# Performance work log

Measured on AMD Instinct MI355X. Metric: run time of the kernel, lower is better.

The kernel has to match this reference:

```python
import jax, jax.numpy as jnp
import numpy as np

D_MODEL = 1024
N_HEADS = 16
HEAD_DIM = D_MODEL // N_HEADS
N_EXPERTS = 4
HIDDEN = 4 * D_MODEL
B, T = 1, 2048


def _apply_rope(x, sin, cos):
    # x: [..., D]; sin/cos broadcastable to [..., D/2]
    x1, x2 = x[..., ::2], x[..., 1::2]
    r1 = x1 * cos - x2 * sin
    r2 = x1 * sin + x2 * cos
    return jnp.stack((r1, r2), axis=-1).reshape(x.shape)


def setup_inputs() -> dict:
    key = jax.random.key(0)
    ks = jax.random.split(key, 16)
    s = 0.02
    d, E, Hd = D_MODEL, N_EXPERTS, HIDDEN
    return {
        "x": jax.random.normal(ks[0], (B, T, d), dtype=jnp.float32),
        "w_dw": jax.random.normal(ks[1], (d, 3), dtype=jnp.float32) * s,      # depthwise conv k=3
        "w_pw": jax.random.normal(ks[2], (d, d), dtype=jnp.float32) * s,      # pointwise conv [out,in]
        "w_qkv": jax.random.normal(ks[3], (3 * d, d), dtype=jnp.float32) * s,  # [out,in]
        "w_o": jax.random.normal(ks[4], (d, d), dtype=jnp.float32) * s,
        "w_gate": jax.random.normal(ks[5], (d, d), dtype=jnp.float32) * s,
        "b_gate": jnp.zeros((d,), dtype=jnp.float32),
        "ln_g": jnp.ones((d,), dtype=jnp.float32),
        "ln_b": jnp.zeros((d,), dtype=jnp.float32),
        "w_moe_gate": jax.random.normal(ks[6], (E, d), dtype=jnp.float32) * s,  # Linear no bias [out,in]
        "w1": jax.random.normal(ks[7], (E, Hd, d), dtype=jnp.float32) * s,
        "b1": jnp.zeros((E, Hd), dtype=jnp.float32),
        "w2": jax.random.normal(ks[8], (E, d, Hd), dtype=jnp.float32) * s,
        "b2": jnp.zeros((E, d), dtype=jnp.float32),
    }


def reference(x, w_dw, w_pw, w_qkv, w_o, w_gate, b_gate, ln_g, ln_b,
              w_moe_gate, w1, b1, w2, b2):
    Bv, Tv, d = x.shape
    H, Dh = N_HEADS, HEAD_DIM
    dt = x.dtype

    # --- causal conv mixer (depthwise k=3, causal left pad 2, then pointwise) ---
    xp = jnp.pad(x, ((0, 0), (2, 0), (0, 0)))
    y = (xp[:, 0:Tv] * w_dw[:, 0] + xp[:, 1:Tv + 1] * w_dw[:, 1]
         + xp[:, 2:Tv + 2] * w_dw[:, 2])
    y = jnp.einsum('btd,ed->bte', y, w_pw)
    x = x + y

    # --- qkv projection + split heads ---
    qkv = jnp.einsum('btd,ed->bte', x, w_qkv).reshape(Bv, Tv, 3, H, Dh)
    q, k, v = qkv[:, :, 0], qkv[:, :, 1], qkv[:, :, 2]

    # --- RoPE (head_dim even) ---
    inv_freq = 1.0 / (10000.0 ** (jnp.arange(0, Dh, 2, dtype=dt) / Dh))
    pos = jnp.arange(Tv, dtype=dt)
    theta = pos[:, None] * inv_freq[None, :]                 # [T, Dh/2]
    sin = jnp.sin(theta)[None, :, None, :]                   # [1,T,1,Dh/2]
    cos = jnp.cos(theta)[None, :, None, :]
    q = _apply_rope(q, sin, cos)
    k = _apply_rope(k, sin, cos)

    # --- linear attention via full kv outer-product cumsum ---
    q_phi = jax.nn.elu(q) + 1.0
    k_phi = jax.nn.elu(k) + 1.0
    kv = k_phi[..., :, None] * v[..., None, :]               # [B,T,H,D,D]
    kv_prefix = jnp.cumsum(kv, axis=1)
    k_prefix = jnp.cumsum(k_phi, axis=1)
    num = jnp.einsum('bthd,bthdm->bthm', q_phi, kv_prefix)
    denom = jnp.sum(q_phi * k_prefix, axis=-1, keepdims=True)
    attn = num / (denom + 1e-6)
    attn = attn.reshape(Bv, Tv, d)
    attn = jnp.einsum('btd,ed->bte', attn, w_o)

    # --- delta-gated residual (dropout = identity in eval) ---
    delta = x - jnp.concatenate([x[:, :1], x[:, :-1]], axis=1)
    gate = jax.nn.sigmoid(jnp.einsum('btd,ed->bte', delta, w_gate) + b_gate)
    x = x + gate * attn

    # --- LayerNorm + dense MoE FFN ---
    mu = jnp.mean(x, axis=-1, keepdims=True)
    var = jnp.mean((x - mu) ** 2, axis=-1, keepdims=True)
    h = (x - mu) / jnp.sqrt(var + 1e-5) * ln_g + ln_b

    gw = jax.nn.softmax(jnp.einsum('btd,ed->bte', h, w_moe_gate), axis=-1)  # [B,T,E]
    hid = jax.nn.silu(jnp.einsum('btd,efd->btef', h, w1) + b1)              # [B,T,E,Hd]
    eo = jnp.einsum('btef,edf->bted', hid, w2) + b2                          # [B,T,E,d]
    ffn = jnp.einsum('bte,bted->btd', gw, eo)
    return x + ffn
```

## Files before the change

### kernel.cpp

```cpp
#include <hip/hip_runtime.h>
#include <hip/hip_bf16.h>

#define TSEQ 2048
#define DM   1024
#define NHD  16
#define DHD  64
#define NEXP 4
#define HIDN 4096
#define NMOE (NEXP*HIDN)
#define CHK  128
#define NCHK (TSEQ/CHK)

typedef __attribute__((ext_vector_type(8))) short          bf16x8_v;
typedef __attribute__((ext_vector_type(4))) float          f32x4_v;
typedef __attribute__((ext_vector_type(4))) unsigned short us4_v;

__device__ __forceinline__ unsigned short bfbits(float f) {
  __hip_bfloat16 h = __float2bfloat16(f);
  return __builtin_bit_cast(unsigned short, h);
}
__device__ __forceinline__ float bf2f(unsigned short u) {
  return __uint_as_float(((unsigned)u) << 16);
}
__device__ __forceinline__ float wave_sum(float v) {
  #pragma unroll
  for (int o = 32; o; o >>= 1) v += __shfl_xor(v, o, 64);
  return v;
}
__device__ __forceinline__ void gl_lds16(const void* g, void* l) {
  __builtin_amdgcn_global_load_lds((const __attribute__((address_space(1))) void*)g,
                                   (__attribute__((address_space(3))) void*)l, 16, 0, 0);
}

__global__ __launch_bounds__(256) void cvt_bf16(const float* __restrict__ in,
                                                unsigned short* __restrict__ out, int n4) {
  int i = blockIdx.x * 256 + threadIdx.x;
  if (i >= n4) return;
  float4 v = ((const float4*)in)[i];
  us4_v o; o.x = bfbits(v.x); o.y = bfbits(v.y); o.z = bfbits(v.z); o.w = bfbits(v.w);
  ((us4_v*)out)[i] = o;
}

__global__ __launch_bounds__(256) void conv_dw(const float* __restrict__ x,
                                               const float* __restrict__ w_dw,
                                               unsigned short* __restrict__ y_bf) {
  int i = blockIdx.x * 256 + threadIdx.x;
  int c = i & (DM - 1);
  int t = i >> 10;
  float a = (t >= 2) ? x[i - 2 * DM] : 0.f;
  float b = (t >= 1) ? x[i - DM]     : 0.f;
  float d = x[i];
  float y = a * w_dw[c * 3] + b * w_dw[c * 3 + 1] + d * w_dw[c * 3 + 2];
  y_bf[i] = bfbits(y);
}

template <int EPI>
__global__ __launch_bounds__(256, 2) void gemm128s(
    const unsigned short* __restrict__ A, const unsigned short* __restrict__ A2,
    const unsigned short* __restrict__ B, const unsigned short* __restrict__ B2,
    float* __restrict__ Cf, float* __restrict__ Cf2,
    unsigned short* __restrict__ Cbf, const float* __restrict__ ex0,
    int lda, int ldb, int K, int ldc)
{
  if (EPI == 0) { if (blockIdx.z) { A = A2; B = B2; Cf = Cf2; } }

  __shared__ unsigned short As[2][128][64];
  __shared__ unsigned short Bs[2][128][64];

  const int nwg = gridDim.x * gridDim.y;
  const int bidl = blockIdx.y * gridDim.x + blockIdx.x;
  const int chunk = nwg >> 3;
  const int swz = (bidl & 7) * chunk + (bidl >> 3);
  const int ntn = gridDim.y;
  const int rest = swz >> 3;
  const int m0 = ((rest / ntn) * 8 + (swz & 7)) << 7;
  const int n0 = (rest % ntn) << 7;

  const int tid = threadIdx.x;
  const int srow = tid >> 3;
  const int scol = (tid & 7) << 3;
  const int scsw = (((tid & 7) ^ ((tid >> 3) & 7)) << 3);
  const unsigned short* gA = A + (size_t)(m0 + srow) * lda + scsw;
  const unsigned short* gB = B + (size_t)(n0 + srow) * ldb + scsw;

  auto stage = [&](int k0, int b) {
    #pragma unroll
    for (int i = 0; i < 4; i++)
      gl_lds16(gA + (size_t)(i * 32) * lda + k0, &As[b][i * 32 + srow][scol]);
    #pragma unroll
    for (int i = 0; i < 4; i++)
      gl_lds16(gB + (size_t)(i * 32) * ldb + k0, &Bs[b][i * 32 + srow][scol]);
  };

  const int lane = tid & 63, wv = tid >> 6;
  const int wr = (wv >> 1) << 6, wc = (wv & 1) << 6;
  const int fr = lane & 15, kreg = lane >> 4, r4 = kreg << 2;
  const int c0 = ((kreg) ^ (lane & 7)) << 3;
  const int c1 = ((4 + kreg) ^ (lane & 7)) << 3;

  f32x4_v acc[4][4] = {};

  stage(0, 0);
  const int nt = K >> 6;
  for (int t = 0; t < nt; t++) {
    const int p = t & 1;
    if (t + 1 < nt) {
      stage((t + 1) << 6, p ^ 1);
      asm volatile("s_waitcnt vmcnt(8)" ::: "memory");
    } else {
      asm volatile("s_waitcnt vmcnt(0)" ::: "memory");
    }
    __builtin_amdgcn_s_barrier();
    __builtin_amdgcn_sched_barrier(0);
    bf16x8_v af[4][2], bfm[4][2];
    #pragma unroll
    for (int m = 0; m < 4; m++) {
      af[m][0] = *(const bf16x8_v*)&As[p][wr + m * 16 + fr][c0];
      af[m][1] = *(const bf16x8_v*)&As[p][wr + m * 16 + fr][c1];
    }
    #pragma unroll
    for (int n = 0; n < 4; n++) {
      bfm[n][0] = *(const bf16x8_v*)&Bs[p][wc + n * 16 + fr][c0];
      bfm[n][1] = *(const bf16x8_v*)&Bs[p][wc + n * 16 + fr][c1];
    }
    __builtin_amdgcn_s_setprio(1);
    #pragma unroll
    for (int m = 0; m < 4; m++)
      #pragma unroll
      for (int n = 0; n < 4; n++) {
        acc[m][n] = __builtin_amdgcn_mfma_f32_16x16x32_bf16(af[m][0], bfm[n][0], acc[m][n], 0, 0, 0);
        acc[m][n] = __builtin_amdgcn_mfma_f32_16x16x32_bf16(af[m][1], bfm[n][1], acc[m][n], 0, 0, 0);
      }
    __builtin_amdgcn_s_setprio(0);
    __builtin_amdgcn_s_barrier();
  }

  #pragma unroll
  for (int m = 0; m < 4; m++)
    #pragma unroll
    for (int n = 0; n < 4; n++)
      #pragma unroll
      for (int j = 0; j < 4; j++) {
        int grow = m0 + wr + m * 16 + r4 + j;
        int gcol = n0 + wc + n * 16 + fr;
        size_t off = (size_t)grow * ldc + gcol;
        if (EPI == 0) {
          Cf[off] = acc[m][n][j];
        } else {
          float s = acc[m][n][j] + ex0[off];
          Cf[off] = s; Cbf[off] = bfbits(s);
        }
      }
}

template <int EPI>
__global__ __launch_bounds__(512, 1) void gemm256(
    const unsigned short* __restrict__ A, const unsigned short* __restrict__ B,
    float* __restrict__ Cf, unsigned short* __restrict__ Cbf,
    const float* __restrict__ ex0, const float* __restrict__ ex1,
    int lda, int ldb, int K, int ldc, int kPerZ)
{
  if (EPI == 1) {
    int ko = blockIdx.z * kPerZ;
    A += ko;
    B += (size_t)(ko >> 12) * DM * HIDN + (ko & 4095);
    K = kPerZ;
  }

  __shared__ unsigned short As[2][256][64];
  __shared__ unsigned short Bs[2][256][64];

  int bidl = blockIdx.y * gridDim.x + blockIdx.x;
  int chunk = (gridDim.x * gridDim.y) >> 3;
  int swz = (bidl & 7) * chunk + (bidl >> 3);
  int m0 = (swz & 7) << 8, n0 = (swz >> 3) << 8;

  const int tid = threadIdx.x;
  const int srow = tid >> 3;
  const int scol = (tid & 7) << 3;
  const int scsw = (((tid & 7) ^ ((tid >> 3) & 7)) << 3);
  const unsigned short* gA = A + (size_t)(m0 + srow) * lda + scsw;
  const unsigned short* gB = B + (size_t)(n0 + srow) * ldb + scsw;

  auto stageA = [&](int k0, int b) {
    #pragma unroll
    for (int i = 0; i < 4; i++)
      gl_lds16(gA + (size_t)(i * 64) * lda + k0, &As[b][i * 64 + srow][scol]);
  };
  auto stageB = [&](int k0, int b) {
    #pragma unroll
    for (int i = 0; i < 4; i++)
      gl_lds16(gB + (size_t)(i * 64) * ldb + k0, &Bs[b][i * 64 + srow][scol]);
  };

  const int lane = tid & 63, wv = tid >> 6;
  const int wm = wv >> 2, wn = wv & 3;
  const int fr = lane & 15;
  const int kreg = lane >> 4, r4 = kreg << 2;
  const int c0 = ((kreg) ^ (lane & 7)) << 3;
  const int c1 = ((4 + kreg) ^ (lane & 7)) << 3;

  f32x4_v acc[8][4] = {};
  bf16x8_v a0[4][2], a1[4][2], bb[2][2];

  stageA(0, 0); stageB(0, 0);
  const int nt = K >> 6;
  for (int t = 0; t < nt; t++) {
    const int p = t & 1;
    if (t + 1 < nt) {
      stageA((t + 1) << 6, p ^ 1);
      asm volatile("s_waitcnt vmcnt(4)" ::: "memory");
    } else {
      asm volatile("s_waitcnt vmcnt(0)" ::: "memory");
    }
    __builtin_amdgcn_s_barrier();
    __builtin_amdgcn_sched_barrier(0);
    #pragma unroll
    for (int m = 0; m < 4; m++) {
      a0[m][0] = *(const bf16x8_v*)&As[p][wm * 128 + m * 16 + fr][c0];
      a0[m][1] = *(const bf16x8_v*)&As[p][wm * 128 + m * 16 + fr][c1];
    }
    #pragma unroll
    for (int n = 0; n < 2; n++) {
      bb[n][0] = *(const bf16x8_v*)&Bs[p][wn * 64 + n * 16 + fr][c0];
      bb[n][1] = *(const bf16x8_v*)&Bs[p][wn * 64 + n * 16 + fr][c1];
    }
    __builtin_amdgcn_s_setprio(1);
    #pragma unroll
    for (int m = 0; m < 4; m++)
      #pragma unroll
      for (int n = 0; n < 2; n++) {
        acc[m][n] = __builtin_amdgcn_mfma_f32_16x16x32_bf16(a0[m][0], bb[n][0], acc[m][n], 0, 0, 0);
        acc[m][n] = __builtin_amdgcn_mfma_f32_16x16x32_bf16(a0[m][1], bb[n][1], acc[m][n], 0, 0, 0);
      }
    __builtin_amdgcn_s_setprio(0);
    #pragma unroll
    for (int m = 0; m < 4; m++) {
      a1[m][0] = *(const bf16x8_v*)&As[p][wm * 128 + 64 + m * 16 + fr][c0];
      a1[m][1] = *(const bf16x8_v*)&As[p][wm * 128 + 64 + m * 16 + fr][c1];
    }
    __builtin_amdgcn_s_setprio(1);
    #pragma unroll
    for (int m = 0; m < 4; m++)
      #pragma unroll
      for (int n = 0; n < 2; n++) {
        acc[m + 4][n] = __builtin_amdgcn_mfma_f32_16x16x32_bf16(a1[m][0], bb[n][0], acc[m + 4][n], 0, 0, 0);
        acc[m + 4][n] = __builtin_amdgcn_mfma_f32_16x16x32_bf16(a1[m][1], bb[n][1], acc[m + 4][n], 0, 0, 0);
      }
    __builtin_amdgcn_s_setprio(0);
    #pragma unroll
    for (int n = 0; n < 2; n++) {
      bb[n][0] = *(const bf16x8_v*)&Bs[p][wn * 64 + 32 + n * 16 + fr][c0];
      bb[n][1] = *(const bf16x8_v*)&Bs[p][wn * 64 + 32 + n * 16 + fr][c1];
    }
    if (t + 1 < nt) stageB((t + 1) << 6, p ^ 1);
    __builtin_amdgcn_s_setprio(1);
    #pragma unroll
    for (int m = 0; m < 4; m++)
      #pragma unroll
      for (int n = 0; n < 2; n++) {
        acc[m][n + 2] = __builtin_amdgcn_mfma_f32_16x16x32_bf16(a0[m][0], bb[n][0], acc[m][n + 2], 0, 0, 0);
        acc[m][n + 2] = __builtin_amdgcn_mfma_f32_16x16x32_bf16(a0[m][1], bb[n][1], acc[m][n + 2], 0, 0, 0);
      }
    #pragma unroll
    for (int m = 0; m < 4; m++)
      #pragma unroll
      for (int n = 0; n < 2; n++) {
        acc[m + 4][n + 2] = __builtin_amdgcn_mfma_f32_16x16x32_bf16(a1[m][0], bb[n][0], acc[m + 4][n + 2], 0, 0, 0);
        acc[m + 4][n + 2] = __builtin_amdgcn_mfma_f32_16x16x32_bf16(a1[m][1], bb[n][1], acc[m + 4][n + 2], 0, 0, 0);
      }
    __builtin_amdgcn_s_setprio(0);
    __builtin_amdgcn_s_barrier();
  }

  #pragma unroll
  for (int m = 0; m < 8; m++)
    #pragma unroll
    for (int n = 0; n < 4; n++)
      #pragma unroll
      for (int j = 0; j < 4; j++) {
        int grow = m0 + wm * 128 + m * 16 + r4 + j;
        int gcol = n0 + wn * 64 + n * 16 + fr;
        size_t off = (size_t)grow * ldc + gcol;
        if (EPI == 0) {
          float c2 = acc[m][n][j] + ex0[gcol];
          float sl = c2 / (1.f + __expf(-c2));
          Cbf[off] = bfbits(sl * ex1[grow * 4 + (gcol >> 12)]);
        } else {
          atomicAdd(&Cf[off], acc[m][n][j]);
        }
      }
}

__global__ __launch_bounds__(256) void rope_phi(const float* __restrict__ qkv,
                                                unsigned short* __restrict__ qphi,
                                                unsigned short* __restrict__ kphi,
                                                unsigned short* __restrict__ vout) {
  int idx = blockIdx.x * 256 + threadIdx.x;
  int i = idx & 31;
  int h = (idx >> 5) & 15;
  int t = idx >> 9;
  const float* row = qkv + (size_t)t * 3 * DM;
  int col = h * 64 + 2 * i;
  float q0 = row[col],          q1 = row[col + 1];
  float k0 = row[DM + col],     k1 = row[DM + col + 1];
  float v0 = row[2 * DM + col], v1 = row[2 * DM + col + 1];
  float invf = __expf(-(float)(2 * i) * (9.210340371976184f / 64.f));
  float th = (float)t * invf;
  float s, c;
  sincosf(th, &s, &c);
  float qr0 = q0 * c - q1 * s, qr1 = q0 * s + q1 * c;
  float kr0 = k0 * c - k1 * s, kr1 = k0 * s + k1 * c;
  size_t o = (size_t)t * DM + col;
  qphi[o]     = bfbits(qr0 > 0.f ? qr0 + 1.f : __expf(qr0));
  qphi[o + 1] = bfbits(qr1 > 0.f ? qr1 + 1.f : __expf(qr1));
  kphi[o]     = bfbits(kr0 > 0.f ? kr0 + 1.f : __expf(kr0));
  kphi[o + 1] = bfbits(kr1 > 0.f ? kr1 + 1.f : __expf(kr1));
  vout[o]     = bfbits(v0);
  vout[o + 1] = bfbits(v1);
}

__global__ __launch_bounds__(256) void kv_chunk(const unsigned short* __restrict__ kphi,
                                                const unsigned short* __restrict__ vbf,
                                                float* __restrict__ kvT,
                                                float* __restrict__ ksbuf) {
  int h = blockIdx.x & 15, c = blockIdx.x >> 4;
  __shared__ unsigned short Kt[64][136];
  __shared__ unsigned short Vt[64][136];
  int tid = threadIdx.x;
  int rr = tid >> 3, cc = (tid & 7) << 3;
  int t0 = c * CHK;
  #pragma unroll
  for (int g = 0; g < 4; g++) {
    int t = g * 32 + rr;
    bf16x8_v k8 = *(const bf16x8_v*)&kphi[(size_t)(t0 + t) * DM + h * 64 + cc];
    bf16x8_v v8 = *(const bf16x8_v*)&vbf [(size_t)(t0 + t) * DM + h * 64 + cc];
    #pragma unroll
    for (int j = 0; j < 8; j++) { Kt[cc + j][t] = (unsigned short)k8[j];
                                  Vt[cc + j][t] = (unsigned short)v8[j]; }
  }
  __syncthreads();
  int lane = tid & 63, wv = tid >> 6;
  int wr = (wv >> 1) << 5, wc = (wv & 1) << 5;
  int fr = lane & 15, fk = (lane >> 4) << 3, r4 = (lane >> 4) << 2;
  f32x4_v acc[2][2] = {};
  #pragma unroll
  for (int k0 = 0; k0 < 128; k0 += 32) {
    bf16x8_v a[2], b[2];
    #pragma unroll
    for (int m = 0; m < 2; m++) a[m] = *(const bf16x8_v*)&Kt[wr + m * 16 + fr][k0 + fk];
    #pragma unroll
    for (int n = 0; n < 2; n++) b[n] = *(const bf16x8_v*)&Vt[wc + n * 16 + fr][k0 + fk];
    #pragma unroll
    for (int m = 0; m < 2; m++)
      #pragma unroll
      for (int n = 0; n < 2; n++)
        acc[m][n] = __builtin_amdgcn_mfma_f32_16x16x32_bf16(a[m], b[n], acc[m][n], 0, 0, 0);
  }
  float* kvout = kvT + (size_t)(h * NCHK + c) * 4096;
  #pragma unroll
  for (int m = 0; m < 2; m++)
    #pragma unroll
    for (int n = 0; n < 2; n++)
      #pragma unroll
      for (int j = 0; j < 4; j++)
        kvout[(wc + n * 16 + fr) * 64 + (wr + m * 16 + r4 + j)] = acc[m][n][j];
  float s = 0.f;
  int d = tid >> 2, q = tid & 3;
  for (int i = 0; i < 32; i++) s += bf2f(Kt[d][q * 32 + i]);
  s += __shfl_xor(s, 1, 64); s += __shfl_xor(s, 2, 64);
  if (q == 0) ksbuf[(h * NCHK + c) * 64 + d] = s;
}

__global__ __launch_bounds__(256) void prefix_kv(const float* __restrict__ kvT,
                                                 const float* __restrict__ ksbuf,
                                                 unsigned short* __restrict__ sT,
                                                 float* __restrict__ kspre) {
  int idx = blockIdx.x * 256 + threadIdx.x;
  int h = idx >> 12, nd = idx & 4095;
  float s = 0.f;
  for (int c = 0; c < NCHK; c++) {
    size_t o = (size_t)(h * NCHK + c) * 4096 + nd;
    sT[o] = bfbits(s);
    s += kvT[o];
  }
  if (idx < NHD * 64) {
    float ks = 0.f;
    for (int c = 0; c < NCHK; c++) {
      int o = ((idx >> 6) * NCHK + c) * 64 + (idx & 63);
      kspre[o] = ks;
      ks += ksbuf[o];
    }
  }
}

__global__ __launch_bounds__(256) void attn_chunk(const unsigned short* __restrict__ qphi,
                                                  const unsigned short* __restrict__ kphi,
                                                  const unsigned short* __restrict__ vbf,
                                                  const unsigned short* __restrict__ sT,
                                                  const float* __restrict__ kspre,
                                                  unsigned short* __restrict__ attn_bf) {
  int h = blockIdx.x & 15, c = blockIdx.x >> 4;
  __shared__ unsigned short Qs[128][72];
  __shared__ unsigned short Ks[128][72];
  __shared__ unsigned short Ms[128][200];
  __shared__ unsigned short Vt[64][200];
  __shared__ float ksL[64];
  __shared__ float denL[128];
  int tid = threadIdx.x;
  int t0 = c * CHK;
  int rr = tid >> 3, cc = (tid & 7) << 3;
  #pragma unroll
  for (int g = 0; g < 4; g++) {
    int t = g * 32 + rr;
    bf16x8_v q8 = *(const bf16x8_v*)&qphi[(size_t)(t0 + t) * DM + h * 64 + cc];
    bf16x8_v k8 = *(const bf16x8_v*)&kphi[(size_t)(t0 + t) * DM + h * 64 + cc];
    bf16x8_v v8 = *(const bf16x8_v*)&vbf [(size_t)(t0 + t) * DM + h * 64 + cc];
    *(bf16x8_v*)&Qs[t][cc] = q8;
    *(bf16x8_v*)&Ks[t][cc] = k8;
    *(bf16x8_v*)&Ms[t][128 + cc] = q8;
    #pragma unroll
    for (int j = 0; j < 8; j++) Vt[cc + j][t] = (unsigned short)v8[j];
  }
  #pragma unroll
  for (int g = 0; g < 2; g++) {
    int e = (g * 256 + tid) * 8;
    bf16x8_v s8 = *(const bf16x8_v*)&sT[(size_t)(h * NCHK + c) * 4096 + e];
    *(bf16x8_v*)&Vt[e >> 6][128 + (e & 63)] = s8;
  }
  if (tid < 64) ksL[tid] = kspre[(h * NCHK + c) * 64 + tid];
  __syncthreads();

  int lane = tid & 63, wv = tid >> 6;
  int wr = (wv >> 1) << 6, wc = (wv & 1) << 6;
  int fr = lane & 15, fk = (lane >> 4) << 3, r4 = (lane >> 4) << 2;
  {
    f32x4_v acc[4][4] = {};
    #pragma unroll
    for (int k0 = 0; k0 < 64; k0 += 32) {
      bf16x8_v a[4], b[4];
      #pragma unroll
      for (int m = 0; m < 4; m++) a[m] = *(const bf16x8_v*)&Qs[wr + m * 16 + fr][k0 + fk];
      #pragma unroll
      for (int n = 0; n < 4; n++) b[n] = *(const bf16x8_v*)&Ks[wc + n * 16 + fr][k0 + fk];
      #pragma unroll
      for (int m = 0; m < 4; m++)
        #pragma unroll
        for (int n = 0; n < 4; n++)
          acc[m][n] = __builtin_amdgcn_mfma_f32_16x16x32_bf16(a[m], b[n], acc[m][n], 0, 0, 0);
    }
    #pragma unroll
    for (int m = 0; m < 4; m++)
      #pragma unroll
      for (int n = 0; n < 4; n++)
        #pragma unroll
        for (int j = 0; j < 4; j++) {
          int r = wr + m * 16 + r4 + j, col = wc + n * 16 + fr;
          Ms[r][col] = bfbits(col <= r ? acc[m][n][j] : 0.f);
        }
  }
  __syncthreads();
  {
    int dr = tid >> 1, half = tid & 1;
    float s = 0.f;
    for (int i = 0; i < 64; i++) s += bf2f(Ms[dr][half * 64 + i]);
    for (int i = 0; i < 32; i++) {
      int d = half * 32 + i;
      s += bf2f(Qs[dr][d]) * ksL[d];
    }
    s += __shfl_xor(s, 1, 64);
    if (!half) denL[dr] = 1.f / (s + 1e-6f);
  }
  __syncthreads();
  {
    int wc2 = (wv & 1) << 5;
    f32x4_v acc[4][2] = {};
    #pragma unroll
    for (int k0 = 0; k0 < 192; k0 += 32) {
      bf16x8_v a[4], b[2];
      #pragma unroll
      for (int m = 0; m < 4; m++) a[m] = *(const bf16x8_v*)&Ms[wr + m * 16 + fr][k0 + fk];
      #pragma unroll
      for (int n = 0; n < 2; n++) b[n] = *(const bf16x8_v*)&Vt[wc2 + n * 16 + fr][k0 + fk];
      #pragma unroll
      for (int m = 0; m < 4; m++)
        #pragma unroll
        for (int n = 0; n < 2; n++)
          acc[m][n] = __builtin_amdgcn_mfma_f32_16x16x32_bf16(a[m], b[n], acc[m][n], 0, 0, 0);
    }
    #pragma unroll
    for (int m = 0; m < 4; m++)
      #pragma unroll
      for (int n = 0; n < 2; n++)
        #pragma unroll
        for (int j = 0; j < 4; j++) {
          int row = wr + m * 16 + r4 + j;
          attn_bf[(size_t)(t0 + row) * DM + h * 64 + wc2 + n * 16 + fr]
              = bfbits(acc[m][n][j] * denL[row]);
        }
  }
}

__global__ __launch_bounds__(256) void delta_cvt(const unsigned short* __restrict__ x1b,
                                                 unsigned short* __restrict__ delta_bf) {
  int i = blockIdx.x * 256 + threadIdx.x;
  int i8 = i * 8;
  int t = i8 >> 10;
  bf16x8_v cur = *(const bf16x8_v*)&x1b[i8];
  bf16x8_v prv = t ? *(const bf16x8_v*)&x1b[i8 - DM] : cur;
  bf16x8_v o;
  #pragma unroll
  for (int j = 0; j < 8; j++)
    o[j] = (short)bfbits(bf2f((unsigned short)cur[j]) - bf2f((unsigned short)prv[j]));
  *(bf16x8_v*)&delta_bf[i8] = o;
}

__global__ __launch_bounds__(256) void fuse_ln(const float* __restrict__ x1,
                                               const float* __restrict__ attn_o,
                                               const float* __restrict__ gate_lin,
                                               const float* __restrict__ b_gate,
                                               const float* __restrict__ ln_g,
                                               const float* __restrict__ ln_b,
                                               const float* __restrict__ w_moe,
                                               float* __restrict__ x2,
                                               unsigned short* __restrict__ h_bf,
                                               float* __restrict__ gw) {
  int t = blockIdx.x;
  int tid = threadIdx.x;
  __shared__ float hrow[DM];
  __shared__ float red[16];
  float vals[4], s = 0.f, s2 = 0.f;
  #pragma unroll
  for (int j = 0; j < 4; j++) {
    int c = tid + j * 256;
    size_t ix = (size_t)t * DM + c;
    float g = gate_lin[ix] + b_gate[c];
    float sig = 1.f / (1.f + __expf(-g));
    float xv = x1[ix] + sig * attn_o[ix];
    x2[ix] = xv; vals[j] = xv; s += xv; s2 += xv * xv;
  }
  s = wave_sum(s); s2 = wave_sum(s2);
  int wvi = tid >> 6, l = tid & 63;
  if (l == 0) { red[wvi] = s; red[4 + wvi] = s2; }
  __syncthreads();
  s  = red[0] + red[1] + red[2] + red[3];
  s2 = red[4] + red[5] + red[6] + red[7];
  float mu = s * (1.f / DM);
  float var = s2 * (1.f / DM) - mu * mu;
  float rstd = rsqrtf(var + 1e-5f);
  #pragma unroll
  for (int j = 0; j < 4; j++) {
    int c = tid + j * 256;
    size_t ix = (size_t)t * DM + c;
    float h = (vals[j] - mu) * rstd * ln_g[c] + ln_b[c];
    h_bf[ix] = bfbits(h); hrow[c] = h;
  }
  __syncthreads();
  float dot = 0.f;
  for (int i0 = l; i0 < DM; i0 += 64) dot += hrow[i0] * w_moe[wvi * DM + i0];
  dot = wave_sum(dot);
  if (l == 0) red[8 + wvi] = dot;
  __syncthreads();
  if (tid == 0) {
    float a0 = red[8], a1 = red[9], a2 = red[10], a3 = red[11];
    float mx = fmaxf(fmaxf(a0, a1), fmaxf(a2, a3));
    float e0 = __expf(a0 - mx), e1 = __expf(a1 - mx), e2 = __expf(a2 - mx), e3 = __expf(a3 - mx);
    float inv = 1.f / (e0 + e1 + e2 + e3);
    gw[t * 4 + 0] = e0 * inv; gw[t * 4 + 1] = e1 * inv;
    gw[t * 4 + 2] = e2 * inv; gw[t * 4 + 3] = e3 * inv;
  }
}

__global__ __launch_bounds__(256) void init_out(const float* __restrict__ x2,
                                                const float* __restrict__ gw,
                                                const float* __restrict__ b2,
                                                float* __restrict__ out) {
  int i = blockIdx.x * 256 + threadIdx.x;
  int i4 = i * 4;
  int t = i4 >> 10, c = i4 & 1023;
  const float* g = gw + t * 4;
  float4 o = *(const float4*)&x2[i4];
  #pragma unroll
  for (int e = 0; e < 4; e++) {
    float ge = g[e];
    float4 b = *(const float4*)&b2[e * DM + c];
    o.x += ge * b.x; o.y += ge * b.y; o.z += ge * b.z; o.w += ge * b.w;
  }
  *(float4*)&out[i4] = o;
}

extern "C" void kernel_launch(void* const* d_in, const int* in_sizes, int n_in,
                              void* d_out, int out_size, void* d_ws, size_t ws_size,
                              hipStream_t stream) {
  const float* x      = (const float*)d_in[0];
  const float* w_dw   = (const float*)d_in[1];
  const float* w_pw   = (const float*)d_in[2];
  const float* w_qkv  = (const float*)d_in[3];
  const float* w_o    = (const float*)d_in[4];
  const float* w_gate = (const float*)d_in[5];
  const float* b_gate = (const float*)d_in[6];
  const float* ln_g   = (const float*)d_in[7];
  const float* ln_b   = (const float*)d_in[8];
  const float* w_moe  = (const float*)d_in[9];
  const float* w1     = (const float*)d_in[10];
  const float* b1     = (const float*)d_in[11];
  const float* w2     = (const float*)d_in[12];
  const float* b2     = (const float*)d_in[13];
  float* out = (float*)d_out;

  char* ws = (char*)d_ws;
  size_t off = 0;
  auto alloc = [&](size_t bytes) -> char* {
    char* p = ws + off; off += (bytes + 255) & ~(size_t)255; return p;
  };
  unsigned short* w_pw_bf   = (unsigned short*)alloc((size_t)DM * DM * 2);
  unsigned short* w_qkv_bf  = (unsigned short*)alloc((size_t)3 * DM * DM * 2);
  unsigned short* w_o_bf    = (unsigned short*)alloc((size_t)DM * DM * 2);
  unsigned short* w_gate_bf = (unsigned short*)alloc((size_t)DM * DM * 2);
  unsigned short* w1_bf     = (unsigned short*)alloc((size_t)NMOE * DM * 2);
  unsigned short* w2_bf     = (unsigned short*)alloc((size_t)NEXP * DM * HIDN * 2);
  float*          x1        = (float*)alloc((size_t)TSEQ * DM * 4);
  unsigned short* x1_bf     = (unsigned short*)alloc((size_t)TSEQ * DM * 2);
  unsigned short* y_bf      = (unsigned short*)alloc((size_t)TSEQ * DM * 2);
  float*          gwb       = (float*)alloc((size_t)TSEQ * NEXP * 4);
  float*          attn_o    = (float*)alloc((size_t)TSEQ * DM * 4);
  unsigned short* delta_bf  = (unsigned short*)alloc((size_t)TSEQ * DM * 2);
  float*          gate_lin  = (float*)alloc((size_t)TSEQ * DM * 4);
  float*          x2        = (float*)alloc((size_t)TSEQ * DM * 4);
  unsigned short* h_bf      = (unsigned short*)alloc((size_t)TSEQ * DM * 2);
  float*          kvT       = (float*)alloc((size_t)NHD * NCHK * 4096 * 4);
  unsigned short* sTb       = (unsigned short*)alloc((size_t)NHD * NCHK * 4096 * 2);
  float*          ksbuf     = (float*)alloc((size_t)NHD * NCHK * 64 * 4);
  float*          kspre     = (float*)alloc((size_t)NHD * NCHK * 64 * 4);
  char*           pool      = alloc((size_t)TSEQ * NMOE * 2);
  if (off > ws_size) return;

  float*          qkv      = (float*)pool;
  unsigned short* qphi     = (unsigned short*)(pool + (size_t)TSEQ * 3 * DM * 4);
  unsigned short* kphi     = qphi + (size_t)TSEQ * DM;
  unsigned short* vbf      = kphi + (size_t)TSEQ * DM;
  unsigned short* attn_bf  = vbf + (size_t)TSEQ * DM;
  unsigned short* hids     = (unsigned short*)pool;

  cvt_bf16<<<1024,  256, 0, stream>>>(w_pw,   w_pw_bf,   DM * DM / 4);
  cvt_bf16<<<3072,  256, 0, stream>>>(w_qkv,  w_qkv_bf,  3 * DM * DM / 4);
  cvt_bf16<<<1024,  256, 0, stream>>>(w_o,    w_o_bf,    DM * DM / 4);
  cvt_bf16<<<1024,  256, 0, stream>>>(w_gate, w_gate_bf, DM * DM / 4);
  cvt_bf16<<<16384, 256, 0, stream>>>(w1,     w1_bf,     NMOE * DM / 4);
  cvt_bf16<<<16384, 256, 0, stream>>>(w2,     w2_bf,     NEXP * DM * HIDN / 4);

  conv_dw<<<8192, 256, 0, stream>>>(x, w_dw, y_bf);
  gemm128s<1><<<dim3(16, 8, 1), 256, 0, stream>>>(y_bf, nullptr, w_pw_bf, nullptr,
      x1, nullptr, x1_bf, x, DM, DM, DM, DM);

  gemm128s<0><<<dim3(16, 24, 1), 256, 0, stream>>>(x1_bf, nullptr, w_qkv_bf, nullptr,
      qkv, nullptr, nullptr, nullptr, DM, DM, DM, 3 * DM);
  rope_phi<<<4096, 256, 0, stream>>>(qkv, qphi, kphi, vbf);

  kv_chunk<<<NHD * NCHK, 256, 0, stream>>>(kphi, vbf, kvT, ksbuf);
  prefix_kv<<<256, 256, 0, stream>>>(kvT, ksbuf, sTb, kspre);
  attn_chunk<<<NHD * NCHK, 256, 0, stream>>>(qphi, kphi, vbf, sTb, kspre, attn_bf);
  delta_cvt<<<1024, 256, 0, stream>>>(x1_bf, delta_bf);

  gemm128s<0><<<dim3(16, 8, 2), 256, 0, stream>>>(attn_bf, delta_bf, w_o_bf, w_gate_bf,
      attn_o, gate_lin, nullptr, nullptr, DM, DM, DM, DM);

  fuse_ln<<<2048, 256, 0, stream>>>(x1, attn_o, gate_lin, b_gate, ln_g, ln_b, w_moe,
                                    x2, h_bf, gwb);

  init_out<<<2048, 256, 0, stream>>>(x2, gwb, b2, out);
  gemm256<0><<<dim3(8, 64, 1), 512, 0, stream>>>(h_bf, w1_bf, nullptr, hids,
      b1, gwb, DM, DM, DM, NMOE, 0);
  gemm256<1><<<dim3(8, 4, 8), 512, 0, stream>>>(hids, w2_bf, out, nullptr,
      nullptr, nullptr, NMOE, HIDN, NMOE, DM, NMOE / 8);
}
```

Before: 366.2 us.

## Replace 256x256 MoE GEMM tiles with 128x128 tiles at higher occupancy

The two MoE FFN GEMMs move from a 256x256 tile, 512-thread kernel with K-step 64 to a 128x128 tile, 256-thread kernel with K-step 32, launched with four blocks per CU. This gives more workgroups and more waves per CU to hide latency, and uses a simpler single-phase staging and MFMA loop. The cost is lower operand reuse per tile, so more global and LDS traffic per FLOP, more loop iterations, and more atomics in the split-K second GEMM.

```diff
diff --git a/kernel.cpp b/kernel.cpp
--- a/kernel.cpp
+++ b/kernel.cpp
@@ -154,7 +154,7 @@
 }
 
 template <int EPI>
-__global__ __launch_bounds__(512, 1) void gemm256(
+__global__ __launch_bounds__(256, 4) void moe128(
     const unsigned short* __restrict__ A, const unsigned short* __restrict__ B,
     float* __restrict__ Cf, unsigned short* __restrict__ Cbf,
     const float* __restrict__ ex0, const float* __restrict__ ex1,
@@ -167,120 +167,74 @@
     K = kPerZ;
   }
 
-  __shared__ unsigned short As[2][256][64];
-  __shared__ unsigned short Bs[2][256][64];
-
-  int bidl = blockIdx.y * gridDim.x + blockIdx.x;
-  int chunk = (gridDim.x * gridDim.y) >> 3;
-  int swz = (bidl & 7) * chunk + (bidl >> 3);
-  int m0 = (swz & 7) << 8, n0 = (swz >> 3) << 8;
+  __shared__ unsigned short As[2][128][32];
+  __shared__ unsigned short Bs[2][128][32];
+
+  const int nwg = gridDim.x * gridDim.y;
+  const int bidl = blockIdx.y * gridDim.x + blockIdx.x;
+  const int chunk = nwg >> 3;
+  const int swz = (bidl & 7) * chunk + (bidl >> 3);
+  const int ntn = gridDim.y;
+  const int rest = swz >> 3;
+  const int m0 = ((rest / ntn) * 8 + (swz & 7)) << 7;
+  const int n0 = (rest % ntn) << 7;
 
   const int tid = threadIdx.x;
-  const int srow = tid >> 3;
-  const int scol = (tid & 7) << 3;
-  const int scsw = (((tid & 7) ^ ((tid >> 3) & 7)) << 3);
+  const int srow = tid >> 2;
+  const int scol = (tid & 3) << 3;
+  const int scsw = (((tid & 3) ^ ((tid >> 2) & 3)) << 3);
   const unsigned short* gA = A + (size_t)(m0 + srow) * lda + scsw;
   const unsigned short* gB = B + (size_t)(n0 + srow) * ldb + scsw;
 
-  auto stageA = [&](int k0, int b) {
-    #pragma unroll
-    for (int i = 0; i < 4; i++)
-      gl_lds16(gA + (size_t)(i * 64) * lda + k0, &As[b][i * 64 + srow][scol]);
+  auto stage = [&](int k0, int b) {
+    gl_lds16(gA + k0,                     &As[b][srow][scol]);
+    gl_lds16(gA + (size_t)64 * lda + k0,  &As[b][srow + 64][scol]);
+    gl_lds16(gB + k0,                     &Bs[b][srow][scol]);
+    gl_lds16(gB + (size_t)64 * ldb + k0,  &Bs[b][srow + 64][scol]);
   };
-  auto stageB = [&](int k0, int b) {
-    #pragma unroll
-    for (int i = 0; i < 4; i++)
-      gl_lds16(gB + (size_t)(i * 64) * ldb + k0, &Bs[b][i * 64 + srow][scol]);
-  };
 
   const int lane = tid & 63, wv = tid >> 6;
-  const int wm = wv >> 2, wn = wv & 3;
-  const int fr = lane & 15;
-  const int kreg = lane >> 4, r4 = kreg << 2;
-  const int c0 = ((kreg) ^ (lane & 7)) << 3;
-  const int c1 = ((4 + kreg) ^ (lane & 7)) << 3;
-
-  f32x4_v acc[8][4] = {};
-  bf16x8_v a0[4][2], a1[4][2], bb[2][2];
-
-  stageA(0, 0); stageB(0, 0);
-  const int nt = K >> 6;
+  const int wr = (wv >> 1) << 6, wc = (wv & 1) << 6;
+  const int fr = lane & 15, kreg = lane >> 4, r4 = kreg << 2;
+  const int csw = ((kreg ^ (fr & 3)) << 3);
+
+  f32x4_v acc[4][4] = {};
+
+  stage(0, 0);
+  const int nt = K >> 5;
   for (int t = 0; t < nt; t++) {
     const int p = t & 1;
     if (t + 1 < nt) {
-      stageA((t + 1) << 6, p ^ 1);
+      stage((t + 1) << 5, p ^ 1);
       asm volatile("s_waitcnt vmcnt(4)" ::: "memory");
     } else {
       asm volatile("s_waitcnt vmcnt(0)" ::: "memory");
     }
     __builtin_amdgcn_s_barrier();
     __builtin_amdgcn_sched_barrier(0);
-    #pragma unroll
-    for (int m = 0; m < 4; m++) {
-      a0[m][0] = *(const bf16x8_v*)&As[p][wm * 128 + m * 16 + fr][c0];
-      a0[m][1] = *(const bf16x8_v*)&As[p][wm * 128 + m * 16 + fr][c1];
-    }
-    #pragma unroll
-    for (int n = 0; n < 2; n++) {
-      bb[n][0] = *(const bf16x8_v*)&Bs[p][wn * 64 + n * 16 + fr][c0];
-      bb[n][1] = *(const bf16x8_v*)&Bs[p][wn * 64 + n * 16 + fr][c1];
-    }
+    bf16x8_v af[4], bfm[4];
+    #pragma unroll
+    for (int m = 0; m < 4; m++) af[m]  = *(const bf16x8_v*)&As[p][wr + m * 16 + fr][csw];
+    #pragma unroll
+    for (int n = 0; n < 4; n++) bfm[n] = *(const bf16x8_v*)&Bs[p][wc + n * 16 + fr][csw];
     __builtin_amdgcn_s_setprio(1);
     #pragma unroll
     for (int m = 0; m < 4; m++)
       #pragma unroll
-      for (int n = 0; n < 2; n++) {
-        acc[m][n] = __builtin_amdgcn_mfma_f32_16x16x32_bf16(a0[m][0], bb[n][0], acc[m][n], 0, 0, 0);
-        acc[m][n] = __builtin_amdgcn_mfma_f32_16x16x32_bf16(a0[m][1], bb[n][1], acc[m][n], 0, 0, 0);
-      }
-    __builtin_amdgcn_s_setprio(0);
-    #pragma unroll
-    for (int m = 0; m < 4; m++) {
-      a1[m][0] = *(const bf16x8_v*)&As[p][wm * 128 + 64 + m * 16 + fr][c0];
-      a1[m][1] = *(const bf16x8_v*)&As[p][wm * 128 + 64 + m * 16 + fr][c1];
-    }
-    __builtin_amdgcn_s_setprio(1);
-    #pragma unroll
-    for (int m = 0; m < 4; m++)
-      #pragma unroll
-      for (int n = 0; n < 2; n++) {
-        acc[m + 4][n] = __builtin_amdgcn_mfma_f32_16x16x32_bf16(a1[m][0], bb[n][0], acc[m + 4][n], 0, 0, 0);
-        acc[m + 4][n] = __builtin_amdgcn_mfma_f32_16x16x32_bf16(a1[m][1], bb[n][1], acc[m + 4][n], 0, 0, 0);
-      }
-    __builtin_amdgcn_s_setprio(0);
-    #pragma unroll
-    for (int n = 0; n < 2; n++) {
-      bb[n][0] = *(const bf16x8_v*)&Bs[p][wn * 64 + 32 + n * 16 + fr][c0];
-      bb[n][1] = *(const bf16x8_v*)&Bs[p][wn * 64 + 32 + n * 16 + fr][c1];
-    }
-    if (t + 1 < nt) stageB((t + 1) << 6, p ^ 1);
-    __builtin_amdgcn_s_setprio(1);
-    #pragma unroll
-    for (int m = 0; m < 4; m++)
-      #pragma unroll
-      for (int n = 0; n < 2; n++) {
-        acc[m][n + 2] = __builtin_amdgcn_mfma_f32_16x16x32_bf16(a0[m][0], bb[n][0], acc[m][n + 2], 0, 0, 0);
-        acc[m][n + 2] = __builtin_amdgcn_mfma_f32_16x16x32_bf16(a0[m][1], bb[n][1], acc[m][n + 2], 0, 0, 0);
-      }
-    #pragma unroll
-    for (int m = 0; m < 4; m++)
-      #pragma unroll
-      for (int n = 0; n < 2; n++) {
-        acc[m + 4][n + 2] = __builtin_amdgcn_mfma_f32_16x16x32_bf16(a1[m][0], bb[n][0], acc[m + 4][n + 2], 0, 0, 0);
-        acc[m + 4][n + 2] = __builtin_amdgcn_mfma_f32_16x16x32_bf16(a1[m][1], bb[n][1], acc[m + 4][n + 2], 0, 0, 0);
-      }
+      for (int n = 0; n < 4; n++)
+        acc[m][n] = __builtin_amdgcn_mfma_f32_16x16x32_bf16(af[m], bfm[n], acc[m][n], 0, 0, 0);
     __builtin_amdgcn_s_setprio(0);
     __builtin_amdgcn_s_barrier();
   }
 
   #pragma unroll
-  for (int m = 0; m < 8; m++)
+  for (int m = 0; m < 4; m++)
     #pragma unroll
     for (int n = 0; n < 4; n++)
       #pragma unroll
       for (int j = 0; j < 4; j++) {
-        int grow = m0 + wm * 128 + m * 16 + r4 + j;
-        int gcol = n0 + wn * 64 + n * 16 + fr;
+        int grow = m0 + wr + m * 16 + r4 + j;
+        int gcol = n0 + wc + n * 16 + fr;
         size_t off = (size_t)grow * ldc + gcol;
         if (EPI == 0) {
           float c2 = acc[m][n][j] + ex0[gcol];
@@ -669,8 +623,8 @@
                                     x2, h_bf, gwb);
 
   init_out<<<2048, 256, 0, stream>>>(x2, gwb, b2, out);
-  gemm256<0><<<dim3(8, 64, 1), 512, 0, stream>>>(h_bf, w1_bf, nullptr, hids,
+  moe128<0><<<dim3(16, 128, 1), 256, 0, stream>>>(h_bf, w1_bf, nullptr, hids,
       b1, gwb, DM, DM, DM, NMOE, 0);
-  gemm256<1><<<dim3(8, 4, 8), 512, 0, stream>>>(hids, w2_bf, out, nullptr,
+  moe128<1><<<dim3(16, 8, 8), 256, 0, stream>>>(hids, w2_bf, out, nullptr,
       nullptr, nullptr, NMOE, HIDN, NMOE, DM, NMOE / 8);
 }
```

Result: slower. 383.4 us (+4.7%).

## Fuse fp32-to-bf16 weight conversion into MoE GEMM loads and merge small kernels

Applied to the files above, without the earlier changes.

The two large MoE GEMMs now read fp32 w1/w2 directly, convert them to bf16 in registers and write them into swizzled LDS. This removes the separate conversion passes over the expert weights and their bf16 copies. The four remaining weight conversions are merged into one launch, and init_out is folded into the LayerNorm kernel, which drops the x2 buffer. In exchange, B traffic inside the GEMMs doubles, the B path loses async global-to-LDS loads, and each iteration now ends with a full vmcnt/lgkmcnt wait, which may cut load/compute overlap.

```diff
diff --git a/kernel.cpp b/kernel.cpp
--- a/kernel.cpp
+++ b/kernel.cpp
@@ -32,10 +32,18 @@
                                    (__attribute__((address_space(3))) void*)l, 16, 0, 0);
 }
 
-__global__ __launch_bounds__(256) void cvt_bf16(const float* __restrict__ in,
-                                                unsigned short* __restrict__ out, int n4) {
-  int i = blockIdx.x * 256 + threadIdx.x;
-  if (i >= n4) return;
+__global__ __launch_bounds__(256) void cvt_all(
+    const float* __restrict__ a, unsigned short* __restrict__ oa,
+    const float* __restrict__ b, unsigned short* __restrict__ ob,
+    const float* __restrict__ c, unsigned short* __restrict__ oc,
+    const float* __restrict__ d, unsigned short* __restrict__ od) {
+  int blk = blockIdx.x;
+  const float* in; unsigned short* out; int base;
+  if (blk < 1024)      { in = a; out = oa; base = blk; }
+  else if (blk < 4096) { in = b; out = ob; base = blk - 1024; }
+  else if (blk < 5120) { in = c; out = oc; base = blk - 4096; }
+  else                 { in = d; out = od; base = blk - 5120; }
+  int i = base * 256 + threadIdx.x;
   float4 v = ((const float4*)in)[i];
   us4_v o; o.x = bfbits(v.x); o.y = bfbits(v.y); o.z = bfbits(v.z); o.w = bfbits(v.w);
   ((us4_v*)out)[i] = o;
@@ -155,15 +163,15 @@
 
 template <int EPI>
 __global__ __launch_bounds__(512, 1) void gemm256(
-    const unsigned short* __restrict__ A, const unsigned short* __restrict__ B,
+    const unsigned short* __restrict__ A, const float* __restrict__ Bf,
     float* __restrict__ Cf, unsigned short* __restrict__ Cbf,
     const float* __restrict__ ex0, const float* __restrict__ ex1,
-    int lda, int ldb, int K, int ldc, int kPerZ)
+    int lda, int ldbf, int K, int ldc, int kPerZ)
 {
   if (EPI == 1) {
     int ko = blockIdx.z * kPerZ;
-    A += ko;
-    B += (size_t)(ko >> 12) * DM * HIDN + (ko & 4095);
+    A  += ko;
+    Bf += (size_t)(ko >> 12) * DM * HIDN + (ko & 4095);
     K = kPerZ;
   }
 
@@ -180,17 +188,31 @@
   const int scol = (tid & 7) << 3;
   const int scsw = (((tid & 7) ^ ((tid >> 3) & 7)) << 3);
   const unsigned short* gA = A + (size_t)(m0 + srow) * lda + scsw;
-  const unsigned short* gB = B + (size_t)(n0 + srow) * ldb + scsw;
+
+  const int br = tid >> 1, bc = (tid & 1) << 5;
+  const float* gBf = Bf + (size_t)(n0 + br) * ldbf + bc;
 
   auto stageA = [&](int k0, int b) {
     #pragma unroll
     for (int i = 0; i < 4; i++)
       gl_lds16(gA + (size_t)(i * 64) * lda + k0, &As[b][i * 64 + srow][scol]);
   };
-  auto stageB = [&](int k0, int b) {
-    #pragma unroll
-    for (int i = 0; i < 4; i++)
-      gl_lds16(gB + (size_t)(i * 64) * ldb + k0, &Bs[b][i * 64 + srow][scol]);
+  float4 bl[8];
+  auto loadB = [&](int k0) {
+    #pragma unroll
+    for (int j = 0; j < 8; j++) bl[j] = *(const float4*)(gBf + k0 + j * 4);
+  };
+  auto writeB = [&](int b) {
+    #pragma unroll
+    for (int j = 0; j < 4; j++) {
+      bf16x8_v w;
+      w[0] = (short)bfbits(bl[2*j].x);   w[1] = (short)bfbits(bl[2*j].y);
+      w[2] = (short)bfbits(bl[2*j].z);   w[3] = (short)bfbits(bl[2*j].w);
+      w[4] = (short)bfbits(bl[2*j+1].x); w[5] = (short)bfbits(bl[2*j+1].y);
+      w[6] = (short)bfbits(bl[2*j+1].z); w[7] = (short)bfbits(bl[2*j+1].w);
+      int slot = (((bc >> 3) + j) ^ (br & 7)) << 3;
+      *(bf16x8_v*)&Bs[b][br][slot] = w;
+    }
   };
 
   const int lane = tid & 63, wv = tid >> 6;
@@ -203,18 +225,18 @@
   f32x4_v acc[8][4] = {};
   bf16x8_v a0[4][2], a1[4][2], bb[2][2];
 
-  stageA(0, 0); stageB(0, 0);
+  loadB(0); stageA(0, 0); writeB(0);
+  asm volatile("s_waitcnt vmcnt(0)" ::: "memory");
+  asm volatile("s_waitcnt lgkmcnt(0)" ::: "memory");
+  __builtin_amdgcn_s_barrier();
+  __builtin_amdgcn_sched_barrier(0);
+
   const int nt = K >> 6;
   for (int t = 0; t < nt; t++) {
     const int p = t & 1;
-    if (t + 1 < nt) {
-      stageA((t + 1) << 6, p ^ 1);
-      asm volatile("s_waitcnt vmcnt(4)" ::: "memory");
-    } else {
-      asm volatile("s_waitcnt vmcnt(0)" ::: "memory");
-    }
-    __builtin_amdgcn_s_barrier();
-    __builtin_amdgcn_sched_barrier(0);
+    const bool pf = (t + 1 < nt);
+    const int kn = (t + 1) << 6;
+    if (pf) { loadB(kn); stageA(kn, p ^ 1); }
     #pragma unroll
     for (int m = 0; m < 4; m++) {
       a0[m][0] = *(const bf16x8_v*)&As[p][wm * 128 + m * 16 + fr][c0];
@@ -253,7 +275,6 @@
       bb[n][0] = *(const bf16x8_v*)&Bs[p][wn * 64 + 32 + n * 16 + fr][c0];
       bb[n][1] = *(const bf16x8_v*)&Bs[p][wn * 64 + 32 + n * 16 + fr][c1];
     }
-    if (t + 1 < nt) stageB((t + 1) << 6, p ^ 1);
     __builtin_amdgcn_s_setprio(1);
     #pragma unroll
     for (int m = 0; m < 4; m++)
@@ -270,7 +291,11 @@
         acc[m + 4][n + 2] = __builtin_amdgcn_mfma_f32_16x16x32_bf16(a1[m][1], bb[n][1], acc[m + 4][n + 2], 0, 0, 0);
       }
     __builtin_amdgcn_s_setprio(0);
+    if (pf) writeB(p ^ 1);
+    asm volatile("s_waitcnt vmcnt(0)" ::: "memory");
+    asm volatile("s_waitcnt lgkmcnt(0)" ::: "memory");
     __builtin_amdgcn_s_barrier();
+    __builtin_amdgcn_sched_barrier(0);
   }
 
   #pragma unroll
@@ -522,7 +547,8 @@
                                                const float* __restrict__ ln_g,
                                                const float* __restrict__ ln_b,
                                                const float* __restrict__ w_moe,
-                                               float* __restrict__ x2,
+                                               const float* __restrict__ b2,
+                                               float* __restrict__ out,
                                                unsigned short* __restrict__ h_bf,
                                                float* __restrict__ gw) {
   int t = blockIdx.x;
@@ -537,7 +563,7 @@
     float g = gate_lin[ix] + b_gate[c];
     float sig = 1.f / (1.f + __expf(-g));
     float xv = x1[ix] + sig * attn_o[ix];
-    x2[ix] = xv; vals[j] = xv; s += xv; s2 += xv * xv;
+    vals[j] = xv; s += xv; s2 += xv * xv;
   }
   s = wave_sum(s); s2 = wave_sum(s2);
   int wvi = tid >> 6, l = tid & 63;
@@ -561,32 +587,20 @@
   dot = wave_sum(dot);
   if (l == 0) red[8 + wvi] = dot;
   __syncthreads();
+  float a0 = red[8], a1 = red[9], a2 = red[10], a3 = red[11];
+  float mx = fmaxf(fmaxf(a0, a1), fmaxf(a2, a3));
+  float e0 = __expf(a0 - mx), e1 = __expf(a1 - mx), e2 = __expf(a2 - mx), e3 = __expf(a3 - mx);
+  float inv = 1.f / (e0 + e1 + e2 + e3);
+  float g0 = e0 * inv, g1 = e1 * inv, g2 = e2 * inv, g3 = e3 * inv;
   if (tid == 0) {
-    float a0 = red[8], a1 = red[9], a2 = red[10], a3 = red[11];
-    float mx = fmaxf(fmaxf(a0, a1), fmaxf(a2, a3));
-    float e0 = __expf(a0 - mx), e1 = __expf(a1 - mx), e2 = __expf(a2 - mx), e3 = __expf(a3 - mx);
-    float inv = 1.f / (e0 + e1 + e2 + e3);
-    gw[t * 4 + 0] = e0 * inv; gw[t * 4 + 1] = e1 * inv;
-    gw[t * 4 + 2] = e2 * inv; gw[t * 4 + 3] = e3 * inv;
-  }
-}
-
-__global__ __launch_bounds__(256) void init_out(const float* __restrict__ x2,
-                                                const float* __restrict__ gw,
-                                                const float* __restrict__ b2,
-                                                float* __restrict__ out) {
-  int i = blockIdx.x * 256 + threadIdx.x;
-  int i4 = i * 4;
-  int t = i4 >> 10, c = i4 & 1023;
-  const float* g = gw + t * 4;
-  float4 o = *(const float4*)&x2[i4];
-  #pragma unroll
-  for (int e = 0; e < 4; e++) {
-    float ge = g[e];
-    float4 b = *(const float4*)&b2[e * DM + c];
-    o.x += ge * b.x; o.y += ge * b.y; o.z += ge * b.z; o.w += ge * b.w;
-  }
-  *(float4*)&out[i4] = o;
+    gw[t * 4 + 0] = g0; gw[t * 4 + 1] = g1; gw[t * 4 + 2] = g2; gw[t * 4 + 3] = g3;
+  }
+  #pragma unroll
+  for (int j = 0; j < 4; j++) {
+    int c = tid + j * 256;
+    out[(size_t)t * DM + c] = vals[j] + g0 * b2[c] + g1 * b2[DM + c]
+                            + g2 * b2[2 * DM + c] + g3 * b2[3 * DM + c];
+  }
 }
 
 extern "C" void kernel_launch(void* const* d_in, const int* in_sizes, int n_in,
@@ -617,8 +631,6 @@
   unsigned short* w_qkv_bf  = (unsigned short*)alloc((size_t)3 * DM * DM * 2);
   unsigned short* w_o_bf    = (unsigned short*)alloc((size_t)DM * DM * 2);
   unsigned short* w_gate_bf = (unsigned short*)alloc((size_t)DM * DM * 2);
-  unsigned short* w1_bf     = (unsigned short*)alloc((size_t)NMOE * DM * 2);
-  unsigned short* w2_bf     = (unsigned short*)alloc((size_t)NEXP * DM * HIDN * 2);
   float*          x1        = (float*)alloc((size_t)TSEQ * DM * 4);
   unsigned short* x1_bf     = (unsigned short*)alloc((size_t)TSEQ * DM * 2);
   unsigned short* y_bf      = (unsigned short*)alloc((size_t)TSEQ * DM * 2);
@@ -626,7 +638,6 @@
   float*          attn_o    = (float*)alloc((size_t)TSEQ * DM * 4);
   unsigned short* delta_bf  = (unsigned short*)alloc((size_t)TSEQ * DM * 2);
   float*          gate_lin  = (float*)alloc((size_t)TSEQ * DM * 4);
-  float*          x2        = (float*)alloc((size_t)TSEQ * DM * 4);
   unsigned short* h_bf      = (unsigned short*)alloc((size_t)TSEQ * DM * 2);
   float*          kvT       = (float*)alloc((size_t)NHD * NCHK * 4096 * 4);
   unsigned short* sTb       = (unsigned short*)alloc((size_t)NHD * NCHK * 4096 * 2);
@@ -642,12 +653,8 @@
   unsigned short* attn_bf  = vbf + (size_t)TSEQ * DM;
   unsigned short* hids     = (unsigned short*)pool;
 
-  cvt_bf16<<<1024,  256, 0, stream>>>(w_pw,   w_pw_bf,   DM * DM / 4);
-  cvt_bf16<<<3072,  256, 0, stream>>>(w_qkv,  w_qkv_bf,  3 * DM * DM / 4);
-  cvt_bf16<<<1024,  256, 0, stream>>>(w_o,    w_o_bf,    DM * DM / 4);
-  cvt_bf16<<<1024,  256, 0, stream>>>(w_gate, w_gate_bf, DM * DM / 4);
-  cvt_bf16<<<16384, 256, 0, stream>>>(w1,     w1_bf,     NMOE * DM / 4);
-  cvt_bf16<<<16384, 256, 0, stream>>>(w2,     w2_bf,     NEXP * DM * HIDN / 4);
+  cvt_all<<<6144, 256, 0, stream>>>(w_pw, w_pw_bf, w_qkv, w_qkv_bf,
+                                    w_o, w_o_bf, w_gate, w_gate_bf);
 
   conv_dw<<<8192, 256, 0, stream>>>(x, w_dw, y_bf);
   gemm128s<1><<<dim3(16, 8, 1), 256, 0, stream>>>(y_bf, nullptr, w_pw_bf, nullptr,
@@ -666,11 +673,10 @@
       attn_o, gate_lin, nullptr, nullptr, DM, DM, DM, DM);
 
   fuse_ln<<<2048, 256, 0, stream>>>(x1, attn_o, gate_lin, b_gate, ln_g, ln_b, w_moe,
-                                    x2, h_bf, gwb);
-
-  init_out<<<2048, 256, 0, stream>>>(x2, gwb, b2, out);
-  gemm256<0><<<dim3(8, 64, 1), 512, 0, stream>>>(h_bf, w1_bf, nullptr, hids,
+                                    b2, out, h_bf, gwb);
+
+  gemm256<0><<<dim3(8, 64, 1), 512, 0, stream>>>(h_bf, w1, nullptr, hids,
       b1, gwb, DM, DM, DM, NMOE, 0);
-  gemm256<1><<<dim3(8, 4, 8), 512, 0, stream>>>(hids, w2_bf, out, nullptr,
+  gemm256<1><<<dim3(8, 4, 8), 512, 0, stream>>>(hids, w2, out, nullptr,
       nullptr, nullptr, NMOE, HIDN, NMOE, DM, NMOE / 8);
 }
```

New measurement: 463.1 us. +26.5%, slower.
